# Kernel tuning notes

Measured on AMD Instinct MI355X. Metric: run time of the kernel, lower is better.

Reference implementation:

```python
import jax, jax.numpy as jnp
import numpy as np

SIGMA = 1.0
NDCG_AT_K = 10
EPS = 1e-8


def setup_inputs() -> dict:
    key = jax.random.key(0)
    k1, k2 = jax.random.split(key)
    B, N = 64, 1024
    scores = jax.random.normal(k1, (B, N), dtype=jnp.float32)
    relevances = jax.random.randint(k2, (B, N), 0, 2, dtype=jnp.int32)
    return {"scores": scores, "relevances": relevances}


def reference(scores, relevances):
    # scores: [B, N] float, relevances: [B, N] binary int
    B, N = scores.shape
    y = relevances.astype(jnp.float32)
    rel = y > 0          # [B, N] relevant items (i indices)
    nonrel = y == 0      # [B, N] non-relevant items (j indices)

    pos = jnp.arange(N, dtype=jnp.float32)
    disc = 1.0 / jnp.log2(pos + 2.0)  # DCG discount per position index

    # Ideal DCG@k: sort relevances descending, discounted sum of top-k
    y_sorted = -jnp.sort(-y, axis=-1)
    idcg = jnp.sum(y_sorted[:, :NDCG_AT_K] * disc[:NDCG_AT_K], axis=-1)  # [B]

    # Batches with no rel, no non-rel, or zero idcg are skipped (contribute 0 pairs)
    valid_b = rel.any(axis=-1) & nonrel.any(axis=-1) & (idcg > 0)

    pair_mask = rel[:, :, None] & nonrel[:, None, :] & valid_b[:, None, None]  # [B,N,N]

    # |Delta NDCG| for swapping positions i and j (binary gains 1 vs 0)
    delta = jnp.abs(disc[None, :] - disc[:, None])[None, :, :] / (idcg[:, None, None] + EPS)

    s_diff = scores[:, :, None] - scores[:, None, :]  # [B, N, N]
    pair_loss = delta * jax.nn.softplus(-SIGMA * s_diff)

    total = jnp.sum(jnp.where(pair_mask, pair_loss, 0.0))
    num_pairs = jnp.sum(pair_mask)
    # reduction == 'mean': global mean over all pairs across the batch
    loss = jnp.where(num_pairs > 0, total / num_pairs.astype(jnp.float32), 0.0)
    return loss
```

## Files before the change

kernel.cpp:

```cpp
#include <hip/hip_runtime.h>


#define NPOS  1024
#define SPLIT 16
#define KTOP  10
#define EPSF  1e-8f
#define NCHUNK (NPOS / 64)

__device__ __forceinline__ float softplus_f(float z) {
    return fmaxf(z, 0.0f) + __logf(1.0f + __expf(-fabsf(z)));
}

__global__ __launch_bounds__(256) void lr_pair_kernel(
    const float* __restrict__ scores,
    const int*   __restrict__ relev,
    double*      __restrict__ partials,
    unsigned int* __restrict__ pairCnt)
{
    __shared__ float2 rel2[NPOS];
    __shared__ float2 non2[NPOS];
    __shared__ int    cnt[NCHUNK];
    __shared__ double wsum[4];

    const int b     = blockIdx.x / SPLIT;
    const int slice = blockIdx.x % SPLIT;
    const int tid   = threadIdx.x;
    const int lane  = tid & 63;
    const int wave  = tid >> 6;

    const float* srow = scores + (size_t)b * NPOS;
    const int*   rrow = relev  + (size_t)b * NPOS;

    float sv[4], dv[4];
    int   rposv[4];
    bool  rf[4];
    #pragma unroll
    for (int it = 0; it < 4; ++it) {
        const int c   = it * 4 + wave;
        const int idx = c * 64 + lane;
        sv[it] = srow[idx];
        dv[it] = 1.0f / log2f((float)idx + 2.0f);
        const bool r = rrow[idx] > 0;
        rf[it] = r;
        unsigned long long m = __ballot(r);
        rposv[it] = __popcll(m & ((1ull << lane) - 1ull));
        if (lane == 0) cnt[c] = __popcll(m);
    }
    __syncthreads();

    #pragma unroll
    for (int it = 0; it < 4; ++it) {
        const int c = it * 4 + wave;
        int rbase = 0;
        for (int cc = 0; cc < c; ++cc) rbase += cnt[cc];
        const int nbase = c * 64 - rbase;
        if (rf[it]) rel2[rbase + rposv[it]]          = make_float2(sv[it], dv[it]);
        else        non2[nbase + (lane - rposv[it])] = make_float2(sv[it], dv[it]);
    }
    __syncthreads();

    int nrel = 0;
    #pragma unroll
    for (int c = 0; c < NCHUNK; ++c) nrel += cnt[c];
    const int nnon = NPOS - nrel;

    double block_total = 0.0;
    if (nrel > 0 && nnon > 0) {
        float idcg = 0.0f;
        const int kk = min(nrel, KTOP);
        for (int p = 0; p < kk; ++p) idcg += 1.0f / log2f((float)p + 2.0f);
        const float inv_idcg = 1.0f / (idcg + EPSF);

        for (int k = tid; k < nrel; k += 256) rel2[k].y *= inv_idcg;
        for (int k = tid; k < nnon; k += 256) non2[k].y *= inv_idcg;
        __syncthreads();

        const int i0 = (slice * nrel) / SPLIT;
        const int i1 = ((slice + 1) * nrel) / SPLIT;

        float acc = 0.0f;
        int i = i0;
        for (; i + 4 <= i1; i += 4) {
            const float2 a0 = rel2[i], a1 = rel2[i+1], a2 = rel2[i+2], a3 = rel2[i+3];
            for (int j = tid; j < nnon; j += 256) {
                const float2 bj = non2[j];
                acc += fabsf(a0.y - bj.y) * softplus_f(bj.x - a0.x);
                acc += fabsf(a1.y - bj.y) * softplus_f(bj.x - a1.x);
                acc += fabsf(a2.y - bj.y) * softplus_f(bj.x - a2.x);
                acc += fabsf(a3.y - bj.y) * softplus_f(bj.x - a3.x);
            }
        }
        for (; i < i1; ++i) {
            const float2 a0 = rel2[i];
            for (int j = tid; j < nnon; j += 256) {
                const float2 bj = non2[j];
                acc += fabsf(a0.y - bj.y) * softplus_f(bj.x - a0.x);
            }
        }

        #pragma unroll
        for (int off = 32; off >= 1; off >>= 1) acc += __shfl_down(acc, off);
        if (lane == 0) wsum[wave] = (double)acc;
        __syncthreads();
        if (tid == 0) block_total = wsum[0] + wsum[1] + wsum[2] + wsum[3];
    }

    if (tid == 0) {
        partials[blockIdx.x] = block_total;
        if (slice == 0)
            pairCnt[b] = (nrel > 0 && nnon > 0) ? (unsigned int)(nrel * nnon) : 0u;
    }
}

__global__ __launch_bounds__(256) void lr_final_kernel(
    const double*       __restrict__ partials,
    const unsigned int* __restrict__ pairCnt,
    float*              __restrict__ out,
    int B, int nparts)
{
    __shared__ double    dsh[4];
    __shared__ long long psh[4];

    const int tid = threadIdx.x, lane = tid & 63, wave = tid >> 6;

    double tot = 0.0;
    for (int k = tid; k < nparts; k += 256) tot += partials[k];
    long long pairs = (tid < B) ? (long long)pairCnt[tid] : 0;

    #pragma unroll
    for (int off = 32; off >= 1; off >>= 1) {
        tot   += __shfl_down(tot, off);
        pairs += __shfl_down(pairs, off);
    }
    if (lane == 0) { dsh[wave] = tot; psh[wave] = pairs; }
    __syncthreads();
    if (tid == 0) {
        double    tt = dsh[0] + dsh[1] + dsh[2] + dsh[3];
        long long np = psh[0] + psh[1] + psh[2] + psh[3];
        out[0] = (np > 0) ? (float)(tt / (double)np) : 0.0f;
    }
}

extern "C" void kernel_launch(void* const* d_in, const int* in_sizes, int n_in,
                              void* d_out, int out_size, void* d_ws, size_t ws_size,
                              hipStream_t stream) {
    const float* scores = (const float*)d_in[0];
    const int*   relev  = (const int*)d_in[1];
    float*       out    = (float*)d_out;
    const int    B      = in_sizes[0] / NPOS;
    const int    nparts = B * SPLIT;

    double*       partials = (double*)d_ws;
    unsigned int* pairCnt  = (unsigned int*)(partials + nparts);

    lr_pair_kernel<<<nparts, 256, 0, stream>>>(scores, relev, partials, pairCnt);
    lr_final_kernel<<<1, 256, 0, stream>>>(partials, pairCnt, out, B, nparts);
}
```

Before: 76.14 us.

## Split row partitioning into its own kernel and fuse final reduction via last-block atomic

Before, each of the 16 slice blocks per row redid the full ballot-based partition and idcg scaling. Now a separate per-row kernel does this once and writes compacted relevant and non-relevant arrays to workspace. The pair kernel loads these into shared memory, uses four independent accumulators, and has the last finishing block do the global reduction through an atomic counter, which removes the separate final-kernel launch. In exchange it adds a global-memory round trip, a dependent launch, and a larger workspace (the pairs read assumes B <= 64).

After: 90.85 us. 1.19x slower.

```diff
diff --git a/kernel.cpp b/kernel.cpp
--- a/kernel.cpp
+++ b/kernel.cpp
@@ -1,47 +1,41 @@
 #include <hip/hip_runtime.h>
 
 
-#define NPOS  1024
-#define SPLIT 16
-#define KTOP  10
-#define EPSF  1e-8f
-#define NCHUNK (NPOS / 64)
+#define NPOS   1024
+#define NCHUNK 16
+#define KTOP   10
+#define EPSF   1e-8f
+#define SPLIT2 16
+#define MAXB   64
 
 __device__ __forceinline__ float softplus_f(float z) {
     return fmaxf(z, 0.0f) + __logf(1.0f + __expf(-fabsf(z)));
 }
 
-__global__ __launch_bounds__(256) void lr_pair_kernel(
+__global__ __launch_bounds__(256) void lr_partition_kernel(
     const float* __restrict__ scores,
     const int*   __restrict__ relev,
-    double*      __restrict__ partials,
-    unsigned int* __restrict__ pairCnt)
+    float2*      __restrict__ relC,
+    float2*      __restrict__ nonC,
+    int*         __restrict__ nrelArr,
+    unsigned*    __restrict__ pairsArr,
+    unsigned*    __restrict__ done)
 {
     __shared__ float2 rel2[NPOS];
     __shared__ float2 non2[NPOS];
     __shared__ int    cnt[NCHUNK];
-    __shared__ double wsum[4];
 
-    const int b     = blockIdx.x / SPLIT;
-    const int slice = blockIdx.x % SPLIT;
-    const int tid   = threadIdx.x;
-    const int lane  = tid & 63;
-    const int wave  = tid >> 6;
-
+    const int b = blockIdx.x, tid = threadIdx.x, lane = tid & 63, wave = tid >> 6;
     const float* srow = scores + (size_t)b * NPOS;
     const int*   rrow = relev  + (size_t)b * NPOS;
 
-    float sv[4], dv[4];
-    int   rposv[4];
-    bool  rf[4];
+    float sv[4], dv[4]; int rposv[4]; bool rf[4];
     #pragma unroll
     for (int it = 0; it < 4; ++it) {
-        const int c   = it * 4 + wave;
-        const int idx = c * 64 + lane;
+        const int c = it * 4 + wave, idx = c * 64 + lane;
         sv[it] = srow[idx];
         dv[it] = 1.0f / log2f((float)idx + 2.0f);
-        const bool r = rrow[idx] > 0;
-        rf[it] = r;
+        const bool r = rrow[idx] > 0; rf[it] = r;
         unsigned long long m = __ballot(r);
         rposv[it] = __popcll(m & ((1ull << lane) - 1ull));
         if (lane == 0) cnt[c] = __popcll(m);
@@ -64,39 +58,71 @@
     for (int c = 0; c < NCHUNK; ++c) nrel += cnt[c];
     const int nnon = NPOS - nrel;
 
+    float idcg = 0.0f;
+    const int kk = min(nrel, KTOP);
+    for (int p = 0; p < kk; ++p) idcg += 1.0f / log2f((float)p + 2.0f);
+    const float inv = 1.0f / (idcg + EPSF);
+
+    for (int k = tid; k < nrel; k += 256) { float2 v = rel2[k]; v.y *= inv; relC[(size_t)b*NPOS + k] = v; }
+    for (int k = tid; k < nnon; k += 256) { float2 v = non2[k]; v.y *= inv; nonC[(size_t)b*NPOS + k] = v; }
+
+    if (tid == 0) {
+        nrelArr[b]  = nrel;
+        pairsArr[b] = (nrel > 0 && nnon > 0) ? (unsigned)(nrel * nnon) : 0u;
+        if (b == 0) done[0] = 0u;
+    }
+}
+
+__global__ __launch_bounds__(256) void lr_pair_kernel(
+    const float2*   __restrict__ relC,
+    const float2*   __restrict__ nonC,
+    const int*      __restrict__ nrelArr,
+    const unsigned* __restrict__ pairsArr,
+    double*         __restrict__ partials,
+    unsigned*       __restrict__ done,
+    float*          __restrict__ out,
+    int nblocks)
+{
+    __shared__ float2 nshr[NPOS];
+    __shared__ float2 rshr[64];
+    __shared__ double wsum[4];
+    __shared__ int    lastFlag;
+
+    const int b = blockIdx.x / SPLIT2, slice = blockIdx.x % SPLIT2;
+    const int tid = threadIdx.x, lane = tid & 63, wave = tid >> 6;
+
+    const int nrel = nrelArr[b];
+    const int nnon = NPOS - nrel;
+    const int i0 = (slice * nrel) / SPLIT2;
+    const int i1 = ((slice + 1) * nrel) / SPLIT2;
+    const int ni = i1 - i0;
+
     double block_total = 0.0;
-    if (nrel > 0 && nnon > 0) {
-        float idcg = 0.0f;
-        const int kk = min(nrel, KTOP);
-        for (int p = 0; p < kk; ++p) idcg += 1.0f / log2f((float)p + 2.0f);
-        const float inv_idcg = 1.0f / (idcg + EPSF);
-
-        for (int k = tid; k < nrel; k += 256) rel2[k].y *= inv_idcg;
-        for (int k = tid; k < nnon; k += 256) non2[k].y *= inv_idcg;
+    if (nrel > 0 && nnon > 0 && ni > 0) {
+        for (int k = tid; k < nnon; k += 256) nshr[k] = nonC[(size_t)b*NPOS + k];
+        for (int k = tid; k < ni;   k += 256) rshr[k] = relC[(size_t)b*NPOS + i0 + k];
         __syncthreads();
 
-        const int i0 = (slice * nrel) / SPLIT;
-        const int i1 = ((slice + 1) * nrel) / SPLIT;
-
-        float acc = 0.0f;
-        int i = i0;
-        for (; i + 4 <= i1; i += 4) {
-            const float2 a0 = rel2[i], a1 = rel2[i+1], a2 = rel2[i+2], a3 = rel2[i+3];
+        float acc0 = 0.f, acc1 = 0.f, acc2 = 0.f, acc3 = 0.f;
+        int i = 0;
+        for (; i + 4 <= ni; i += 4) {
+            const float2 a0 = rshr[i], a1 = rshr[i+1], a2 = rshr[i+2], a3 = rshr[i+3];
             for (int j = tid; j < nnon; j += 256) {
-                const float2 bj = non2[j];
-                acc += fabsf(a0.y - bj.y) * softplus_f(bj.x - a0.x);
-                acc += fabsf(a1.y - bj.y) * softplus_f(bj.x - a1.x);
-                acc += fabsf(a2.y - bj.y) * softplus_f(bj.x - a2.x);
-                acc += fabsf(a3.y - bj.y) * softplus_f(bj.x - a3.x);
+                const float2 bj = nshr[j];
+                acc0 += fabsf(a0.y - bj.y) * softplus_f(bj.x - a0.x);
+                acc1 += fabsf(a1.y - bj.y) * softplus_f(bj.x - a1.x);
+                acc2 += fabsf(a2.y - bj.y) * softplus_f(bj.x - a2.x);
+                acc3 += fabsf(a3.y - bj.y) * softplus_f(bj.x - a3.x);
             }
         }
-        for (; i < i1; ++i) {
-            const float2 a0 = rel2[i];
+        for (; i < ni; ++i) {
+            const float2 a0 = rshr[i];
             for (int j = tid; j < nnon; j += 256) {
-                const float2 bj = non2[j];
-                acc += fabsf(a0.y - bj.y) * softplus_f(bj.x - a0.x);
+                const float2 bj = nshr[j];
+                acc0 += fabsf(a0.y - bj.y) * softplus_f(bj.x - a0.x);
             }
         }
+        float acc = (acc0 + acc1) + (acc2 + acc3);
 
         #pragma unroll
         for (int off = 32; off >= 1; off >>= 1) acc += __shfl_down(acc, off);
@@ -106,38 +132,35 @@
     }
 
     if (tid == 0) {
-        partials[blockIdx.x] = block_total;
-        if (slice == 0)
-            pairCnt[b] = (nrel > 0 && nnon > 0) ? (unsigned int)(nrel * nnon) : 0u;
+        __hip_atomic_store(&partials[blockIdx.x], block_total,
+                           __ATOMIC_RELEASE, __HIP_MEMORY_SCOPE_AGENT);
+        unsigned old = __hip_atomic_fetch_add(done, 1u,
+                           __ATOMIC_ACQ_REL, __HIP_MEMORY_SCOPE_AGENT);
+        lastFlag = (old == (unsigned)(nblocks - 1)) ? 1 : 0;
     }
-}
+    __syncthreads();
 
-__global__ __launch_bounds__(256) void lr_final_kernel(
-    const double*       __restrict__ partials,
-    const unsigned int* __restrict__ pairCnt,
-    float*              __restrict__ out,
-    int B, int nparts)
-{
-    __shared__ double    dsh[4];
-    __shared__ long long psh[4];
+    if (lastFlag) {
+        double tot = 0.0;
+        for (int k = tid; k < nblocks; k += 256)
+            tot += __hip_atomic_load(&partials[k],
+                       __ATOMIC_ACQUIRE, __HIP_MEMORY_SCOPE_AGENT);
+        long long pairs = (tid < MAXB) ? (long long)pairsArr[tid] : 0;
 
-    const int tid = threadIdx.x, lane = tid & 63, wave = tid >> 6;
-
-    double tot = 0.0;
-    for (int k = tid; k < nparts; k += 256) tot += partials[k];
-    long long pairs = (tid < B) ? (long long)pairCnt[tid] : 0;
-
-    #pragma unroll
-    for (int off = 32; off >= 1; off >>= 1) {
-        tot   += __shfl_down(tot, off);
-        pairs += __shfl_down(pairs, off);
-    }
-    if (lane == 0) { dsh[wave] = tot; psh[wave] = pairs; }
-    __syncthreads();
-    if (tid == 0) {
-        double    tt = dsh[0] + dsh[1] + dsh[2] + dsh[3];
-        long long np = psh[0] + psh[1] + psh[2] + psh[3];
-        out[0] = (np > 0) ? (float)(tt / (double)np) : 0.0f;
+        #pragma unroll
+        for (int off = 32; off >= 1; off >>= 1) {
+            tot   += __shfl_down(tot, off);
+            pairs += __shfl_down(pairs, off);
+        }
+        __shared__ double    dsh[4];
+        __shared__ long long psh[4];
+        if (lane == 0) { dsh[wave] = tot; psh[wave] = pairs; }
+        __syncthreads();
+        if (tid == 0) {
+            double    tt = dsh[0] + dsh[1] + dsh[2] + dsh[3];
+            long long np = psh[0] + psh[1] + psh[2] + psh[3];
+            out[0] = (np > 0) ? (float)(tt / (double)np) : 0.0f;
+        }
     }
 }
 
@@ -148,11 +171,17 @@
     const int*   relev  = (const int*)d_in[1];
     float*       out    = (float*)d_out;
     const int    B      = in_sizes[0] / NPOS;
-    const int    nparts = B * SPLIT;
+    const int    nblocks = B * SPLIT2;
 
-    double*       partials = (double*)d_ws;
-    unsigned int* pairCnt  = (unsigned int*)(partials + nparts);
+    float2*   relC     = (float2*)d_ws;
+    float2*   nonC     = relC + (size_t)MAXB * NPOS;
+    int*      nrelArr  = (int*)(nonC + (size_t)MAXB * NPOS);
+    unsigned* pairsArr = (unsigned*)(nrelArr + MAXB);
+    double*   partials = (double*)(pairsArr + MAXB);
+    unsigned* done     = (unsigned*)(partials + nblocks);
 
-    lr_pair_kernel<<<nparts, 256, 0, stream>>>(scores, relev, partials, pairCnt);
-    lr_final_kernel<<<1, 256, 0, stream>>>(partials, pairCnt, out, B, nparts);
+    lr_partition_kernel<<<B, 256, 0, stream>>>(scores, relev, relC, nonC,
+                                               nrelArr, pairsArr, done);
+    lr_pair_kernel<<<nblocks, 256, 0, stream>>>(relC, nonC, nrelArr, pairsArr,
+                                                partials, done, out, nblocks);
 }
```
